# Kernel optimization log

Hardware: AMD Instinct MI355X
Metric: run time of the kernel (lower is better)

Reference implementation:

```python
import jax, jax.numpy as jnp
import numpy as np

T, D, F, FS, E = 2048, 1024, 2048, 2048, 8
TOP_K = 1


def setup_inputs() -> dict:
    key = jax.random.key(0)
    ks = jax.random.split(key, 8)
    sd = 1.0 / np.sqrt(D)
    sf = 1.0 / np.sqrt(F)
    sfs = 1.0 / np.sqrt(FS)
    return {
        "hidden_states": jax.random.normal(ks[0], (T, D), jnp.float32),
        "router_w": jax.random.normal(ks[1], (E, D), jnp.float32) * sd,     # Linear(D->E), no bias
        "w_gate": jax.random.normal(ks[2], (E, D, F), jnp.float32) * sd,    # fused gate half
        "w_up": jax.random.normal(ks[3], (E, D, F), jnp.float32) * sd,      # fused up half
        "w_down": jax.random.normal(ks[4], (E, F, D), jnp.float32) * sf,
        "ws_gate": jax.random.normal(ks[5], (D, FS), jnp.float32) * sd,
        "ws_up": jax.random.normal(ks[6], (D, FS), jnp.float32) * sd,
        "ws_down": jax.random.normal(ks[7], (FS, D), jnp.float32) * sfs,
    }


def reference(hidden_states, router_w, w_gate, w_up, w_down, ws_gate, ws_up, ws_down):
    # Router: logits -> top-k -> sigmoid of top-k values (Llama4RenormalizeMoeRoutingMethod)
    logits = hidden_states @ router_w.T                      # [T, E]
    top_vals, top_idx = jax.lax.top_k(logits, TOP_K)         # [T, K]
    scores = jax.nn.sigmoid(top_vals.astype(jnp.float32)).astype(hidden_states.dtype)
    # Combine weights [T, E]; apply_router_weight_on_input=True -> scale INPUT per routed copy
    combine = (jax.nn.one_hot(top_idx, E, dtype=hidden_states.dtype) * scores[..., None]).sum(axis=1)
    xe = combine.T[:, :, None] * hidden_states[None]          # [E, T, D] (zero for non-routed tokens)
    g = jnp.einsum('etd,edf->etf', xe, w_gate)
    u = jnp.einsum('etd,edf->etf', xe, w_up)
    routed = jnp.einsum('etf,efd->etd', jax.nn.silu(g) * u, w_down).sum(axis=0)  # [T, D]
    # Shared expert (GatedMLP, SiLU)
    shared = (jax.nn.silu(hidden_states @ ws_gate) * (hidden_states @ ws_up)) @ ws_down
    return shared + routed
```

## Files before the change

kernel.cpp:

```cpp
#include <hip/hip_runtime.h>
#include <hip/hip_bf16.h>
#include <cstdint>
#include <cstddef>

#define T_TOK 2048
#define DIM   1024
#define FDIM  2048
#define NEXP  8
#define BSTRIDE 40

#define GU_MAX 96
#define DN_MAX 96

typedef short  short8  __attribute__((ext_vector_type(8)));
typedef float  floatx4 __attribute__((ext_vector_type(4)));

__device__ inline unsigned short f2bf(float f) {
    unsigned int u = __builtin_bit_cast(unsigned int, f);
    unsigned int r = (u + 0x7FFFu + ((u >> 16) & 1u)) >> 16;
    return (unsigned short)r;
}

__global__ __launch_bounds__(256) void k_router(
    const float* __restrict__ h, const float* __restrict__ rw,
    int* __restrict__ counts, int* __restrict__ lists,
    unsigned short* __restrict__ hb, unsigned short* __restrict__ xb)
{
    int w = threadIdx.x >> 6, lane = threadIdx.x & 63;
    int t = blockIdx.x * 4 + w;
    const float* hrow = h + (size_t)t * DIM;
    float hv[16];
    #pragma unroll
    for (int i = 0; i < 16; ++i) hv[i] = hrow[lane + 64 * i];
    float acc[NEXP];
    #pragma unroll
    for (int e = 0; e < NEXP; ++e) {
        const float* r = rw + (size_t)e * DIM;
        float s = 0.f;
        #pragma unroll
        for (int i = 0; i < 16; ++i) s += hv[i] * r[lane + 64 * i];
        acc[e] = s;
    }
    #pragma unroll
    for (int e = 0; e < NEXP; ++e) {
        float s = acc[e];
        for (int off = 32; off > 0; off >>= 1) s += __shfl_down(s, off);
        acc[e] = s;
    }
    float score = 0.f;
    if (lane == 0) {
        int be = 0; float bv = acc[0];
        #pragma unroll
        for (int e = 1; e < NEXP; ++e) if (acc[e] > bv) { bv = acc[e]; be = e; }
        score = 1.f / (1.f + __expf(-bv));
        int pos = atomicAdd(&counts[be], 1);
        lists[be * T_TOK + pos] = t;
    }
    score = __shfl(score, 0);
    unsigned short* hbr = hb + (size_t)t * DIM;
    unsigned short* xbr = xb + (size_t)t * DIM;
    #pragma unroll
    for (int i = 0; i < 16; ++i) {
        hbr[lane + 64 * i] = f2bf(hv[i]);
        xbr[lane + 64 * i] = f2bf(score * hv[i]);
    }
}

__global__ void k_schedule(const int* __restrict__ counts,
                           int* __restrict__ gu, int* __restrict__ dn)
{
    if (threadIdx.x != 0 || blockIdx.x != 0) return;
    int n = 0;
    for (int e = 0; e < NEXP; ++e) {
        int c = counts[e];
        for (int r = 0; r < c; r += 64) gu[n++] = (e << 16) | r;
    }
    for (int r = 0; r < T_TOK; r += 64) gu[n++] = (NEXP << 16) | r;
    while (n < GU_MAX) gu[n++] = -1;
    n = 0;
    for (int e = 0; e < NEXP; ++e) {
        int c = counts[e];
        for (int r = 0; r < c; r += 64) {
            dn[n++] = (e << 16) | r;
            dn[n++] = (1 << 28) | (e << 16) | r;
        }
    }
    while (n < DN_MAX) dn[n++] = -1;
}

__global__ __launch_bounds__(256) void k_gateup(
    const unsigned short* __restrict__ xb, const unsigned short* __restrict__ hb,
    const float* __restrict__ w_gate, const float* __restrict__ w_up,
    const float* __restrict__ ws_gate, const float* __restrict__ ws_up,
    const int* __restrict__ counts, const int* __restrict__ lists,
    const int* __restrict__ gu_tiles, unsigned short* __restrict__ Hc)
{
    int ent = gu_tiles[blockIdx.y];
    if (ent < 0) return;
    int e = ent >> 16, row0 = ent & 0xffff;
    bool sh = (e == NEXP);
    int cnt = sh ? T_TOK : counts[e];
    const unsigned short* Asrc = sh ? hb : xb;
    const float* Bg = sh ? ws_gate : w_gate + (size_t)e * DIM * FDIM;
    const float* Bu = sh ? ws_up   : w_up   + (size_t)e * DIM * FDIM;
    int outoff = sh ? FDIM : 0;
    int col0 = blockIdx.x * 128;

    __shared__ int toks[64];
    __shared__ __align__(16) unsigned short As [64  * BSTRIDE];
    __shared__ __align__(16) unsigned short Bgs[128 * BSTRIDE];
    __shared__ __align__(16) unsigned short Bus[128 * BSTRIDE];

    int tid = threadIdx.x;
    if (tid < 64) {
        int r = row0 + tid;
        toks[tid] = (r < cnt) ? (sh ? r : lists[e * T_TOK + r]) : -1;
    }
    __syncthreads();

    int lane = tid & 63, w = tid >> 6;
    int wm = w >> 1, wn = w & 1;
    int arow = tid >> 2, aq = tid & 3;
    int atok = toks[arow];

    floatx4 accg[2][4], accu[2][4];
    #pragma unroll
    for (int mi = 0; mi < 2; ++mi)
    #pragma unroll
    for (int ni = 0; ni < 4; ++ni) {
        floatx4 z = {0.f, 0.f, 0.f, 0.f};
        accg[mi][ni] = z; accu[mi][ni] = z;
    }

    uint4 pa;
    float gr[2][8], ur[2][8];
    auto prefetch = [&](int k0) {
        pa = make_uint4(0u, 0u, 0u, 0u);
        if (atok >= 0) pa = *(const uint4*)(Asrc + (size_t)atok * DIM + k0 + aq * 8);
        #pragma unroll
        for (int it = 0; it < 2; ++it) {
            int tt = tid + it * 256;
            int n = tt & 127, kg = tt >> 7;
            const float* pg = Bg + (size_t)(k0 + kg * 8) * FDIM + col0 + n;
            const float* pu = Bu + (size_t)(k0 + kg * 8) * FDIM + col0 + n;
            #pragma unroll
            for (int j = 0; j < 8; ++j) {
                gr[it][j] = pg[(size_t)j * FDIM];
                ur[it][j] = pu[(size_t)j * FDIM];
            }
        }
    };
    auto commit = [&]() {
        *(uint4*)&As[arow * BSTRIDE + aq * 8] = pa;
        #pragma unroll
        for (int it = 0; it < 2; ++it) {
            int tt = tid + it * 256;
            int n = tt & 127, kg = tt >> 7;
            unsigned int gw[4], uw[4];
            #pragma unroll
            for (int j = 0; j < 4; ++j) {
                gw[j] = (unsigned)f2bf(gr[it][2*j]) | ((unsigned)f2bf(gr[it][2*j+1]) << 16);
                uw[j] = (unsigned)f2bf(ur[it][2*j]) | ((unsigned)f2bf(ur[it][2*j+1]) << 16);
            }
            *(uint4*)&Bgs[n * BSTRIDE + kg * 8] = make_uint4(gw[0], gw[1], gw[2], gw[3]);
            *(uint4*)&Bus[n * BSTRIDE + kg * 8] = make_uint4(uw[0], uw[1], uw[2], uw[3]);
        }
    };

    prefetch(0);
    for (int k0 = 0; k0 < DIM; k0 += 32) {
        __syncthreads();
        commit();
        if (k0 + 32 < DIM) prefetch(k0 + 32);
        __syncthreads();

        int kb = (lane >> 4) * 8;
        short8 a[2], bg[4], bu[4];
        #pragma unroll
        for (int mi = 0; mi < 2; ++mi) {
            int m = wm * 32 + mi * 16 + (lane & 15);
            a[mi] = *(const short8*)&As[m * BSTRIDE + kb];
        }
        #pragma unroll
        for (int ni = 0; ni < 4; ++ni) {
            int n = wn * 64 + ni * 16 + (lane & 15);
            bg[ni] = *(const short8*)&Bgs[n * BSTRIDE + kb];
            bu[ni] = *(const short8*)&Bus[n * BSTRIDE + kb];
        }
        #pragma unroll
        for (int mi = 0; mi < 2; ++mi)
        #pragma unroll
        for (int ni = 0; ni < 4; ++ni) {
            accg[mi][ni] = __builtin_amdgcn_mfma_f32_16x16x32_bf16(a[mi], bg[ni], accg[mi][ni], 0, 0, 0);
            accu[mi][ni] = __builtin_amdgcn_mfma_f32_16x16x32_bf16(a[mi], bu[ni], accu[mi][ni], 0, 0, 0);
        }
    }

    #pragma unroll
    for (int mi = 0; mi < 2; ++mi)
    #pragma unroll
    for (int ni = 0; ni < 4; ++ni)
    #pragma unroll
    for (int r = 0; r < 4; ++r) {
        int row = wm * 32 + mi * 16 + (lane >> 4) * 4 + r;
        int tok = toks[row];
        if (tok < 0) continue;
        int col = col0 + wn * 64 + ni * 16 + (lane & 15);
        float g = accg[mi][ni][r], u = accu[mi][ni][r];
        float hval = (g / (1.f + __expf(-g))) * u;
        Hc[(size_t)tok * (2 * FDIM) + outoff + col] = f2bf(hval);
    }
}

__global__ __launch_bounds__(256) void k_down(
    const unsigned short* __restrict__ Hc,
    const float* __restrict__ w_down, const float* __restrict__ ws_down,
    const int* __restrict__ counts, const int* __restrict__ lists,
    const int* __restrict__ dn_tiles, float* __restrict__ out)
{
    int ent = dn_tiles[blockIdx.y];
    if (ent < 0) return;
    int ks = (ent >> 28) & 1, e = (ent >> 16) & 0xff, row0 = ent & 0xffff;
    int cnt = counts[e];
    const float* B = ks ? ws_down : w_down + (size_t)e * FDIM * DIM;
    int col0 = blockIdx.x * 128;

    __shared__ int toks[64];
    __shared__ __align__(16) unsigned short As[64  * BSTRIDE];
    __shared__ __align__(16) unsigned short Bs[128 * BSTRIDE];

    int tid = threadIdx.x;
    if (tid < 64) {
        int r = row0 + tid;
        toks[tid] = (r < cnt) ? lists[e * T_TOK + r] : -1;
    }
    __syncthreads();

    int lane = tid & 63, w = tid >> 6;
    int wm = w >> 1, wn = w & 1;
    int arow = tid >> 2, aq = tid & 3;
    int atok = toks[arow];
    size_t abase = (size_t)ks * FDIM;

    floatx4 acc[2][4];
    #pragma unroll
    for (int mi = 0; mi < 2; ++mi)
    #pragma unroll
    for (int ni = 0; ni < 4; ++ni) {
        floatx4 z = {0.f, 0.f, 0.f, 0.f};
        acc[mi][ni] = z;
    }

    uint4 pa;
    float br[2][8];
    auto prefetch = [&](int k0) {
        pa = make_uint4(0u, 0u, 0u, 0u);
        if (atok >= 0)
            pa = *(const uint4*)(Hc + (size_t)atok * (2 * FDIM) + abase + k0 + aq * 8);
        #pragma unroll
        for (int it = 0; it < 2; ++it) {
            int tt = tid + it * 256;
            int n = tt & 127, kg = tt >> 7;
            const float* pb = B + (size_t)(k0 + kg * 8) * DIM + col0 + n;
            #pragma unroll
            for (int j = 0; j < 8; ++j) br[it][j] = pb[(size_t)j * DIM];
        }
    };
    auto commit = [&]() {
        *(uint4*)&As[arow * BSTRIDE + aq * 8] = pa;
        #pragma unroll
        for (int it = 0; it < 2; ++it) {
            int tt = tid + it * 256;
            int n = tt & 127, kg = tt >> 7;
            unsigned int bw[4];
            #pragma unroll
            for (int j = 0; j < 4; ++j)
                bw[j] = (unsigned)f2bf(br[it][2*j]) | ((unsigned)f2bf(br[it][2*j+1]) << 16);
            *(uint4*)&Bs[n * BSTRIDE + kg * 8] = make_uint4(bw[0], bw[1], bw[2], bw[3]);
        }
    };

    prefetch(0);
    for (int k0 = 0; k0 < FDIM; k0 += 32) {
        __syncthreads();
        commit();
        if (k0 + 32 < FDIM) prefetch(k0 + 32);
        __syncthreads();

        int kb = (lane >> 4) * 8;
        short8 a[2], b[4];
        #pragma unroll
        for (int mi = 0; mi < 2; ++mi) {
            int m = wm * 32 + mi * 16 + (lane & 15);
            a[mi] = *(const short8*)&As[m * BSTRIDE + kb];
        }
        #pragma unroll
        for (int ni = 0; ni < 4; ++ni) {
            int n = wn * 64 + ni * 16 + (lane & 15);
            b[ni] = *(const short8*)&Bs[n * BSTRIDE + kb];
        }
        #pragma unroll
        for (int mi = 0; mi < 2; ++mi)
        #pragma unroll
        for (int ni = 0; ni < 4; ++ni)
            acc[mi][ni] = __builtin_amdgcn_mfma_f32_16x16x32_bf16(a[mi], b[ni], acc[mi][ni], 0, 0, 0);
    }

    #pragma unroll
    for (int mi = 0; mi < 2; ++mi)
    #pragma unroll
    for (int ni = 0; ni < 4; ++ni)
    #pragma unroll
    for (int r = 0; r < 4; ++r) {
        int row = wm * 32 + mi * 16 + (lane >> 4) * 4 + r;
        int tok = toks[row];
        if (tok < 0) continue;
        int col = col0 + wn * 64 + ni * 16 + (lane & 15);
        atomicAdd(&out[(size_t)tok * DIM + col], acc[mi][ni][r]);
    }
}

extern "C" void kernel_launch(void* const* d_in, const int* in_sizes, int n_in,
                              void* d_out, int out_size, void* d_ws, size_t ws_size,
                              hipStream_t stream)
{
    const float* h   = (const float*)d_in[0];
    const float* rw  = (const float*)d_in[1];
    const float* wg  = (const float*)d_in[2];
    const float* wu  = (const float*)d_in[3];
    const float* wd  = (const float*)d_in[4];
    const float* wsg = (const float*)d_in[5];
    const float* wsu = (const float*)d_in[6];
    const float* wsd = (const float*)d_in[7];
    float* out = (float*)d_out;

    char* ws = (char*)d_ws;
    int* counts   = (int*)ws;
    int* gu_tiles = (int*)(ws + 256);
    int* dn_tiles = (int*)(ws + 1024);
    int* lists    = (int*)(ws + 2048);
    unsigned short* hb = (unsigned short*)(ws + 131072);
    unsigned short* xb = hb + (size_t)T_TOK * DIM;
    unsigned short* Hc = xb + (size_t)T_TOK * DIM;

    hipMemsetAsync(counts, 0, 64, stream);
    hipMemsetAsync(out, 0, (size_t)T_TOK * DIM * sizeof(float), stream);
    k_router<<<dim3(T_TOK / 4), 256, 0, stream>>>(h, rw, counts, lists, hb, xb);
    k_schedule<<<dim3(1), 64, 0, stream>>>(counts, gu_tiles, dn_tiles);
    k_gateup<<<dim3(FDIM / 128, GU_MAX), 256, 0, stream>>>(
        xb, hb, wg, wu, wsg, wsu, counts, lists, gu_tiles, Hc);
    k_down<<<dim3(DIM / 128, DN_MAX), 256, 0, stream>>>(
        Hc, wd, wsd, counts, lists, dn_tiles, out);
}
```

Baseline: 415.9 us.

## Pre-convert weights to transposed bf16 and load tiles via global_load_lds

Adds per-call kernels that convert and transpose the fp32 expert and shared weights into bf16 K-contiguous buffers. The GEMM kernels then stream A and B tiles straight into LDS with global_load_lds, using an XOR swizzle instead of padding. The M tile grows from 64 to 128 tokens. The goal is to remove strided fp32 loads and per-tile conversion from the GEMM inner loops and to raise reuse of the weights. In exchange, each call adds an extra full read and write pass over every weight, and the new loop has a single LDS buffer with no overlap between loading and compute.

```diff
diff --git a/kernel.cpp b/kernel.cpp
--- a/kernel.cpp
+++ b/kernel.cpp
@@ -7,10 +7,9 @@
 #define DIM   1024
 #define FDIM  2048
 #define NEXP  8
-#define BSTRIDE 40
-
-#define GU_MAX 96
-#define DN_MAX 96
+
+#define GU_MAX 64
+#define DN_MAX 64
 
 typedef short  short8  __attribute__((ext_vector_type(8)));
 typedef float  floatx4 __attribute__((ext_vector_type(4)));
@@ -21,6 +20,12 @@
     return (unsigned short)r;
 }
 
+__device__ inline void glds16(const void* g, void* l) {
+    __builtin_amdgcn_global_load_lds(
+        (const __attribute__((address_space(1))) unsigned int*)g,
+        (__attribute__((address_space(3))) unsigned int*)l, 16, 0, 0);
+}
+
 __global__ __launch_bounds__(256) void k_router(
     const float* __restrict__ h, const float* __restrict__ rw,
     int* __restrict__ counts, int* __restrict__ lists,
@@ -73,14 +78,14 @@
     int n = 0;
     for (int e = 0; e < NEXP; ++e) {
         int c = counts[e];
-        for (int r = 0; r < c; r += 64) gu[n++] = (e << 16) | r;
-    }
-    for (int r = 0; r < T_TOK; r += 64) gu[n++] = (NEXP << 16) | r;
+        for (int r = 0; r < c; r += 128) gu[n++] = (e << 16) | r;
+    }
+    for (int r = 0; r < T_TOK; r += 128) gu[n++] = (NEXP << 16) | r;
     while (n < GU_MAX) gu[n++] = -1;
     n = 0;
     for (int e = 0; e < NEXP; ++e) {
         int c = counts[e];
-        for (int r = 0; r < c; r += 64) {
+        for (int r = 0; r < c; r += 128) {
             dn[n++] = (e << 16) | r;
             dn[n++] = (1 << 28) | (e << 16) | r;
         }
@@ -88,10 +93,59 @@
     while (n < DN_MAX) dn[n++] = -1;
 }
 
+__global__ __launch_bounds__(256) void k_cvt_gu(
+    const float* __restrict__ wg, const float* __restrict__ wu,
+    const float* __restrict__ wsg, const float* __restrict__ wsu,
+    unsigned short* __restrict__ wgT, unsigned short* __restrict__ wuT,
+    unsigned short* __restrict__ wsgT, unsigned short* __restrict__ wsuT)
+{
+    int z = blockIdx.y;
+    const float* src; unsigned short* dst;
+    if (z < NEXP)        { src = wg + (size_t)z * DIM * FDIM;          dst = wgT + (size_t)z * FDIM * DIM; }
+    else if (z < 2*NEXP) { src = wu + (size_t)(z - NEXP) * DIM * FDIM; dst = wuT + (size_t)(z - NEXP) * FDIM * DIM; }
+    else if (z == 2*NEXP){ src = wsg; dst = wsgT; }
+    else                 { src = wsu; dst = wsuT; }
+    int n  = blockIdx.x * 64 + (threadIdx.x >> 2);
+    int kg = (threadIdx.x & 3) * 8;
+    for (int k0 = 0; k0 < DIM; k0 += 32) {
+        int k = k0 + kg;
+        float v[8];
+        #pragma unroll
+        for (int j = 0; j < 8; ++j) v[j] = src[(size_t)(k + j) * FDIM + n];
+        unsigned int p[4];
+        #pragma unroll
+        for (int j = 0; j < 4; ++j)
+            p[j] = (unsigned)f2bf(v[2*j]) | ((unsigned)f2bf(v[2*j+1]) << 16);
+        *(uint4*)&dst[(size_t)n * DIM + k] = make_uint4(p[0], p[1], p[2], p[3]);
+    }
+}
+
+__global__ __launch_bounds__(256) void k_cvt_dn(
+    const float* __restrict__ wd, const float* __restrict__ wsd,
+    unsigned short* __restrict__ wdT, unsigned short* __restrict__ wsdT)
+{
+    int z = blockIdx.y;
+    const float* src = (z < NEXP) ? wd + (size_t)z * FDIM * DIM : wsd;
+    unsigned short* dst = (z < NEXP) ? wdT + (size_t)z * DIM * FDIM : wsdT;
+    int n  = blockIdx.x * 64 + (threadIdx.x >> 2);
+    int kg = (threadIdx.x & 3) * 8;
+    for (int k0 = 0; k0 < FDIM; k0 += 32) {
+        int k = k0 + kg;
+        float v[8];
+        #pragma unroll
+        for (int j = 0; j < 8; ++j) v[j] = src[(size_t)(k + j) * DIM + n];
+        unsigned int p[4];
+        #pragma unroll
+        for (int j = 0; j < 4; ++j)
+            p[j] = (unsigned)f2bf(v[2*j]) | ((unsigned)f2bf(v[2*j+1]) << 16);
+        *(uint4*)&dst[(size_t)n * FDIM + k] = make_uint4(p[0], p[1], p[2], p[3]);
+    }
+}
+
 __global__ __launch_bounds__(256) void k_gateup(
     const unsigned short* __restrict__ xb, const unsigned short* __restrict__ hb,
-    const float* __restrict__ w_gate, const float* __restrict__ w_up,
-    const float* __restrict__ ws_gate, const float* __restrict__ ws_up,
+    const unsigned short* __restrict__ wgT, const unsigned short* __restrict__ wuT,
+    const unsigned short* __restrict__ wsgT, const unsigned short* __restrict__ wsuT,
     const int* __restrict__ counts, const int* __restrict__ lists,
     const int* __restrict__ gu_tiles, unsigned short* __restrict__ Hc)
 {
@@ -101,18 +155,18 @@
     bool sh = (e == NEXP);
     int cnt = sh ? T_TOK : counts[e];
     const unsigned short* Asrc = sh ? hb : xb;
-    const float* Bg = sh ? ws_gate : w_gate + (size_t)e * DIM * FDIM;
-    const float* Bu = sh ? ws_up   : w_up   + (size_t)e * DIM * FDIM;
+    const unsigned short* Bg = sh ? wsgT : wgT + (size_t)e * FDIM * DIM;
+    const unsigned short* Bu = sh ? wsuT : wuT + (size_t)e * FDIM * DIM;
     int outoff = sh ? FDIM : 0;
     int col0 = blockIdx.x * 128;
 
-    __shared__ int toks[64];
-    __shared__ __align__(16) unsigned short As [64  * BSTRIDE];
-    __shared__ __align__(16) unsigned short Bgs[128 * BSTRIDE];
-    __shared__ __align__(16) unsigned short Bus[128 * BSTRIDE];
+    __shared__ int toks[128];
+    __shared__ __align__(16) unsigned short As [128 * 32];
+    __shared__ __align__(16) unsigned short Bgs[128 * 32];
+    __shared__ __align__(16) unsigned short Bus[128 * 32];
 
     int tid = threadIdx.x;
-    if (tid < 64) {
+    if (tid < 128) {
         int r = row0 + tid;
         toks[tid] = (r < cnt) ? (sh ? r : lists[e * T_TOK + r]) : -1;
     }
@@ -120,89 +174,69 @@
 
     int lane = tid & 63, w = tid >> 6;
     int wm = w >> 1, wn = w & 1;
-    int arow = tid >> 2, aq = tid & 3;
-    int atok = toks[arow];
-
-    floatx4 accg[2][4], accu[2][4];
-    #pragma unroll
-    for (int mi = 0; mi < 2; ++mi)
+
+    int rw_[2], kg_[2], atk[2];
+    #pragma unroll
+    for (int it = 0; it < 2; ++it) {
+        int tt = tid + it * 256;
+        int rr = tt >> 2, sq = tt & 3;
+        rw_[it] = rr;
+        kg_[it] = (sq ^ ((rr >> 1) & 3)) * 8;
+        int tk = toks[rr];
+        atk[it] = tk < 0 ? 0 : tk;
+    }
+
+    floatx4 accg[4][4], accu[4][4];
+    #pragma unroll
+    for (int mi = 0; mi < 4; ++mi)
     #pragma unroll
     for (int ni = 0; ni < 4; ++ni) {
         floatx4 z = {0.f, 0.f, 0.f, 0.f};
         accg[mi][ni] = z; accu[mi][ni] = z;
     }
 
-    uint4 pa;
-    float gr[2][8], ur[2][8];
-    auto prefetch = [&](int k0) {
-        pa = make_uint4(0u, 0u, 0u, 0u);
-        if (atok >= 0) pa = *(const uint4*)(Asrc + (size_t)atok * DIM + k0 + aq * 8);
-        #pragma unroll
-        for (int it = 0; it < 2; ++it) {
-            int tt = tid + it * 256;
-            int n = tt & 127, kg = tt >> 7;
-            const float* pg = Bg + (size_t)(k0 + kg * 8) * FDIM + col0 + n;
-            const float* pu = Bu + (size_t)(k0 + kg * 8) * FDIM + col0 + n;
-            #pragma unroll
-            for (int j = 0; j < 8; ++j) {
-                gr[it][j] = pg[(size_t)j * FDIM];
-                ur[it][j] = pu[(size_t)j * FDIM];
-            }
-        }
-    };
-    auto commit = [&]() {
-        *(uint4*)&As[arow * BSTRIDE + aq * 8] = pa;
-        #pragma unroll
-        for (int it = 0; it < 2; ++it) {
-            int tt = tid + it * 256;
-            int n = tt & 127, kg = tt >> 7;
-            unsigned int gw[4], uw[4];
-            #pragma unroll
-            for (int j = 0; j < 4; ++j) {
-                gw[j] = (unsigned)f2bf(gr[it][2*j]) | ((unsigned)f2bf(gr[it][2*j+1]) << 16);
-                uw[j] = (unsigned)f2bf(ur[it][2*j]) | ((unsigned)f2bf(ur[it][2*j+1]) << 16);
-            }
-            *(uint4*)&Bgs[n * BSTRIDE + kg * 8] = make_uint4(gw[0], gw[1], gw[2], gw[3]);
-            *(uint4*)&Bus[n * BSTRIDE + kg * 8] = make_uint4(uw[0], uw[1], uw[2], uw[3]);
-        }
-    };
-
-    prefetch(0);
     for (int k0 = 0; k0 < DIM; k0 += 32) {
         __syncthreads();
-        commit();
-        if (k0 + 32 < DIM) prefetch(k0 + 32);
+        #pragma unroll
+        for (int it = 0; it < 2; ++it) {
+            int loff = (tid + it * 256) * 8;
+            glds16(Asrc + (size_t)atk[it] * DIM + k0 + kg_[it], &As[loff]);
+            glds16(Bg + (size_t)(col0 + rw_[it]) * DIM + k0 + kg_[it], &Bgs[loff]);
+            glds16(Bu + (size_t)(col0 + rw_[it]) * DIM + k0 + kg_[it], &Bus[loff]);
+        }
         __syncthreads();
 
         int kb = (lane >> 4) * 8;
-        short8 a[2], bg[4], bu[4];
-        #pragma unroll
-        for (int mi = 0; mi < 2; ++mi) {
-            int m = wm * 32 + mi * 16 + (lane & 15);
-            a[mi] = *(const short8*)&As[m * BSTRIDE + kb];
+        short8 af[4], bgf[4], buf_[4];
+        #pragma unroll
+        for (int mi = 0; mi < 4; ++mi) {
+            int r = wm * 64 + mi * 16 + (lane & 15);
+            int slot = (((kb >> 3) ^ ((r >> 1) & 3))) * 8;
+            af[mi] = *(const short8*)&As[r * 32 + slot];
         }
         #pragma unroll
         for (int ni = 0; ni < 4; ++ni) {
             int n = wn * 64 + ni * 16 + (lane & 15);
-            bg[ni] = *(const short8*)&Bgs[n * BSTRIDE + kb];
-            bu[ni] = *(const short8*)&Bus[n * BSTRIDE + kb];
-        }
-        #pragma unroll
-        for (int mi = 0; mi < 2; ++mi)
+            int slot = (((kb >> 3) ^ ((n >> 1) & 3))) * 8;
+            bgf[ni]  = *(const short8*)&Bgs[n * 32 + slot];
+            buf_[ni] = *(const short8*)&Bus[n * 32 + slot];
+        }
+        #pragma unroll
+        for (int mi = 0; mi < 4; ++mi)
         #pragma unroll
         for (int ni = 0; ni < 4; ++ni) {
-            accg[mi][ni] = __builtin_amdgcn_mfma_f32_16x16x32_bf16(a[mi], bg[ni], accg[mi][ni], 0, 0, 0);
-            accu[mi][ni] = __builtin_amdgcn_mfma_f32_16x16x32_bf16(a[mi], bu[ni], accu[mi][ni], 0, 0, 0);
-        }
-    }
-
-    #pragma unroll
-    for (int mi = 0; mi < 2; ++mi)
+            accg[mi][ni] = __builtin_amdgcn_mfma_f32_16x16x32_bf16(af[mi], bgf[ni],  accg[mi][ni], 0, 0, 0);
+            accu[mi][ni] = __builtin_amdgcn_mfma_f32_16x16x32_bf16(af[mi], buf_[ni], accu[mi][ni], 0, 0, 0);
+        }
+    }
+
+    #pragma unroll
+    for (int mi = 0; mi < 4; ++mi)
     #pragma unroll
     for (int ni = 0; ni < 4; ++ni)
     #pragma unroll
     for (int r = 0; r < 4; ++r) {
-        int row = wm * 32 + mi * 16 + (lane >> 4) * 4 + r;
+        int row = wm * 64 + mi * 16 + (lane >> 4) * 4 + r;
         int tok = toks[row];
         if (tok < 0) continue;
         int col = col0 + wn * 64 + ni * 16 + (lane & 15);
@@ -214,7 +248,7 @@
 
 __global__ __launch_bounds__(256) void k_down(
     const unsigned short* __restrict__ Hc,
-    const float* __restrict__ w_down, const float* __restrict__ ws_down,
+    const unsigned short* __restrict__ wdT, const unsigned short* __restrict__ wsdT,
     const int* __restrict__ counts, const int* __restrict__ lists,
     const int* __restrict__ dn_tiles, float* __restrict__ out)
 {
@@ -222,15 +256,16 @@
     if (ent < 0) return;
     int ks = (ent >> 28) & 1, e = (ent >> 16) & 0xff, row0 = ent & 0xffff;
     int cnt = counts[e];
-    const float* B = ks ? ws_down : w_down + (size_t)e * FDIM * DIM;
+    const unsigned short* B = ks ? wsdT : wdT + (size_t)e * DIM * FDIM;
     int col0 = blockIdx.x * 128;
-
-    __shared__ int toks[64];
-    __shared__ __align__(16) unsigned short As[64  * BSTRIDE];
-    __shared__ __align__(16) unsigned short Bs[128 * BSTRIDE];
+    size_t abase = (size_t)ks * FDIM;
+
+    __shared__ int toks[128];
+    __shared__ __align__(16) unsigned short As[128 * 32];
+    __shared__ __align__(16) unsigned short Bs[128 * 32];
 
     int tid = threadIdx.x;
-    if (tid < 64) {
+    if (tid < 128) {
         int r = row0 + tid;
         toks[tid] = (r < cnt) ? lists[e * T_TOK + r] : -1;
     }
@@ -238,81 +273,65 @@
 
     int lane = tid & 63, w = tid >> 6;
     int wm = w >> 1, wn = w & 1;
-    int arow = tid >> 2, aq = tid & 3;
-    int atok = toks[arow];
-    size_t abase = (size_t)ks * FDIM;
-
-    floatx4 acc[2][4];
-    #pragma unroll
-    for (int mi = 0; mi < 2; ++mi)
+
+    int rw_[2], kg_[2], atk[2];
+    #pragma unroll
+    for (int it = 0; it < 2; ++it) {
+        int tt = tid + it * 256;
+        int rr = tt >> 2, sq = tt & 3;
+        rw_[it] = rr;
+        kg_[it] = (sq ^ ((rr >> 1) & 3)) * 8;
+        int tk = toks[rr];
+        atk[it] = tk < 0 ? 0 : tk;
+    }
+
+    floatx4 acc[4][4];
+    #pragma unroll
+    for (int mi = 0; mi < 4; ++mi)
     #pragma unroll
     for (int ni = 0; ni < 4; ++ni) {
         floatx4 z = {0.f, 0.f, 0.f, 0.f};
         acc[mi][ni] = z;
     }
 
-    uint4 pa;
-    float br[2][8];
-    auto prefetch = [&](int k0) {
-        pa = make_uint4(0u, 0u, 0u, 0u);
-        if (atok >= 0)
-            pa = *(const uint4*)(Hc + (size_t)atok * (2 * FDIM) + abase + k0 + aq * 8);
-        #pragma unroll
-        for (int it = 0; it < 2; ++it) {
-            int tt = tid + it * 256;
-            int n = tt & 127, kg = tt >> 7;
-            const float* pb = B + (size_t)(k0 + kg * 8) * DIM + col0 + n;
-            #pragma unroll
-            for (int j = 0; j < 8; ++j) br[it][j] = pb[(size_t)j * DIM];
-        }
-    };
-    auto commit = [&]() {
-        *(uint4*)&As[arow * BSTRIDE + aq * 8] = pa;
-        #pragma unroll
-        for (int it = 0; it < 2; ++it) {
-            int tt = tid + it * 256;
-            int n = tt & 127, kg = tt >> 7;
-            unsigned int bw[4];
-            #pragma unroll
-            for (int j = 0; j < 4; ++j)
-                bw[j] = (unsigned)f2bf(br[it][2*j]) | ((unsigned)f2bf(br[it][2*j+1]) << 16);
-            *(uint4*)&Bs[n * BSTRIDE + kg * 8] = make_uint4(bw[0], bw[1], bw[2], bw[3]);
-        }
-    };
-
-    prefetch(0);
     for (int k0 = 0; k0 < FDIM; k0 += 32) {
         __syncthreads();
-        commit();
-        if (k0 + 32 < FDIM) prefetch(k0 + 32);
+        #pragma unroll
+        for (int it = 0; it < 2; ++it) {
+            int loff = (tid + it * 256) * 8;
+            glds16(Hc + (size_t)atk[it] * (2 * FDIM) + abase + k0 + kg_[it], &As[loff]);
+            glds16(B + (size_t)(col0 + rw_[it]) * FDIM + k0 + kg_[it], &Bs[loff]);
+        }
         __syncthreads();
 
         int kb = (lane >> 4) * 8;
-        short8 a[2], b[4];
-        #pragma unroll
-        for (int mi = 0; mi < 2; ++mi) {
-            int m = wm * 32 + mi * 16 + (lane & 15);
-            a[mi] = *(const short8*)&As[m * BSTRIDE + kb];
+        short8 af[4], bf[4];
+        #pragma unroll
+        for (int mi = 0; mi < 4; ++mi) {
+            int r = wm * 64 + mi * 16 + (lane & 15);
+            int slot = (((kb >> 3) ^ ((r >> 1) & 3))) * 8;
+            af[mi] = *(const short8*)&As[r * 32 + slot];
         }
         #pragma unroll
         for (int ni = 0; ni < 4; ++ni) {
             int n = wn * 64 + ni * 16 + (lane & 15);
-            b[ni] = *(const short8*)&Bs[n * BSTRIDE + kb];
-        }
-        #pragma unroll
-        for (int mi = 0; mi < 2; ++mi)
+            int slot = (((kb >> 3) ^ ((n >> 1) & 3))) * 8;
+            bf[ni] = *(const short8*)&Bs[n * 32 + slot];
+        }
+        #pragma unroll
+        for (int mi = 0; mi < 4; ++mi)
         #pragma unroll
         for (int ni = 0; ni < 4; ++ni)
-            acc[mi][ni] = __builtin_amdgcn_mfma_f32_16x16x32_bf16(a[mi], b[ni], acc[mi][ni], 0, 0, 0);
-    }
-
-    #pragma unroll
-    for (int mi = 0; mi < 2; ++mi)
+            acc[mi][ni] = __builtin_amdgcn_mfma_f32_16x16x32_bf16(af[mi], bf[ni], acc[mi][ni], 0, 0, 0);
+    }
+
+    #pragma unroll
+    for (int mi = 0; mi < 4; ++mi)
     #pragma unroll
     for (int ni = 0; ni < 4; ++ni)
     #pragma unroll
     for (int r = 0; r < 4; ++r) {
-        int row = wm * 32 + mi * 16 + (lane >> 4) * 4 + r;
+        int row = wm * 64 + mi * 16 + (lane >> 4) * 4 + r;
         int tok = toks[row];
         if (tok < 0) continue;
         int col = col0 + wn * 64 + ni * 16 + (lane & 15);
@@ -334,21 +353,32 @@
     const float* wsd = (const float*)d_in[7];
     float* out = (float*)d_out;
 
+    const size_t MB = 1024 * 1024;
     char* ws = (char*)d_ws;
     int* counts   = (int*)ws;
     int* gu_tiles = (int*)(ws + 256);
     int* dn_tiles = (int*)(ws + 1024);
     int* lists    = (int*)(ws + 2048);
-    unsigned short* hb = (unsigned short*)(ws + 131072);
-    unsigned short* xb = hb + (size_t)T_TOK * DIM;
-    unsigned short* Hc = xb + (size_t)T_TOK * DIM;
+    unsigned short* hb  = (unsigned short*)(ws + 131072);
+    unsigned short* xb  = (unsigned short*)(ws + 131072 + 4*MB);
+    unsigned short* Hc  = (unsigned short*)(ws + 131072 + 8*MB);
+    char* W = ws + 131072 + 24 * MB;
+    unsigned short* wgT  = (unsigned short*)(W);
+    unsigned short* wuT  = (unsigned short*)(W + 32*MB);
+    unsigned short* wsgT = (unsigned short*)(W + 64*MB);
+    unsigned short* wsuT = (unsigned short*)(W + 68*MB);
+    unsigned short* wdT  = (unsigned short*)(W);
+    unsigned short* wsdT = (unsigned short*)(W + 32*MB);
 
     hipMemsetAsync(counts, 0, 64, stream);
     hipMemsetAsync(out, 0, (size_t)T_TOK * DIM * sizeof(float), stream);
+    k_cvt_gu<<<dim3(FDIM / 64, 2 * NEXP + 2), 256, 0, stream>>>(
+        wg, wu, wsg, wsu, wgT, wuT, wsgT, wsuT);
     k_router<<<dim3(T_TOK / 4), 256, 0, stream>>>(h, rw, counts, lists, hb, xb);
     k_schedule<<<dim3(1), 64, 0, stream>>>(counts, gu_tiles, dn_tiles);
     k_gateup<<<dim3(FDIM / 128, GU_MAX), 256, 0, stream>>>(
-        xb, hb, wg, wu, wsg, wsu, counts, lists, gu_tiles, Hc);
+        xb, hb, wgT, wuT, wsgT, wsuT, counts, lists, gu_tiles, Hc);
+    k_cvt_dn<<<dim3(DIM / 64, NEXP + 1), 256, 0, stream>>>(wd, wsd, wdT, wsdT);
     k_down<<<dim3(DIM / 128, DN_MAX), 256, 0, stream>>>(
-        Hc, wd, wsd, counts, lists, dn_tiles, out);
-}
+        Hc, wdT, wsdT, counts, lists, dn_tiles, out);
+}
```

New measurement: 531.1 us. 27.7% more time.

## Enlarge M tiles, double-buffer LDS with direct global-to-LDS loads and XOR swizzle

Applied to the files above, without the earlier changes.

Row tiles in the gate/up and down GEMMs grow from 64 to 128 tokens, and the down kernel's column tile shrinks to 64. Each weight tile loaded from global memory is therefore reused across more tokens. LDS becomes double-buffered with one barrier per k-step, activations are copied global-to-LDS with buffer_load...lds, and padded strides are replaced by an XOR swizzle to avoid bank conflicts. The cost is higher register use (launch_bounds 256,2) and more padding waste on small experts. DN_MAX=64 may be too small if routing is very uneven, since small partial tiles per expert could overflow it.

```diff
diff --git a/kernel.cpp b/kernel.cpp
--- a/kernel.cpp
+++ b/kernel.cpp
@@ -7,10 +7,9 @@
 #define DIM   1024
 #define FDIM  2048
 #define NEXP  8
-#define BSTRIDE 40
-
-#define GU_MAX 96
-#define DN_MAX 96
+
+#define GU_MAX 48
+#define DN_MAX 64
 
 typedef short  short8  __attribute__((ext_vector_type(8)));
 typedef float  floatx4 __attribute__((ext_vector_type(4)));
@@ -21,6 +20,17 @@
     return (unsigned short)r;
 }
 
+__device__ inline unsigned int pk2bf(float a, float b) {
+    return (unsigned int)f2bf(a) | ((unsigned int)f2bf(b) << 16);
+}
+
+__device__ inline void glds16(const void* g, const unsigned short* lds_base, int elem_off) {
+    int u = __builtin_amdgcn_readfirstlane(elem_off);
+    __builtin_amdgcn_global_load_lds(
+        (const __attribute__((address_space(1))) unsigned int*)g,
+        (__attribute__((address_space(3))) unsigned int*)(lds_base + u), 16, 0, 0);
+}
+
 __global__ __launch_bounds__(256) void k_router(
     const float* __restrict__ h, const float* __restrict__ rw,
     int* __restrict__ counts, int* __restrict__ lists,
@@ -73,14 +83,14 @@
     int n = 0;
     for (int e = 0; e < NEXP; ++e) {
         int c = counts[e];
-        for (int r = 0; r < c; r += 64) gu[n++] = (e << 16) | r;
-    }
-    for (int r = 0; r < T_TOK; r += 64) gu[n++] = (NEXP << 16) | r;
+        for (int r = 0; r < c; r += 128) gu[n++] = (e << 16) | r;
+    }
+    for (int r = 0; r < T_TOK; r += 128) gu[n++] = (NEXP << 16) | r;
     while (n < GU_MAX) gu[n++] = -1;
     n = 0;
     for (int e = 0; e < NEXP; ++e) {
         int c = counts[e];
-        for (int r = 0; r < c; r += 64) {
+        for (int r = 0; r < c; r += 128) {
             dn[n++] = (e << 16) | r;
             dn[n++] = (1 << 28) | (e << 16) | r;
         }
@@ -88,7 +98,7 @@
     while (n < DN_MAX) dn[n++] = -1;
 }
 
-__global__ __launch_bounds__(256) void k_gateup(
+__global__ __launch_bounds__(256, 2) void k_gateup(
     const unsigned short* __restrict__ xb, const unsigned short* __restrict__ hb,
     const float* __restrict__ w_gate, const float* __restrict__ w_up,
     const float* __restrict__ ws_gate, const float* __restrict__ ws_up,
@@ -106,13 +116,13 @@
     int outoff = sh ? FDIM : 0;
     int col0 = blockIdx.x * 128;
 
-    __shared__ int toks[64];
-    __shared__ __align__(16) unsigned short As [64  * BSTRIDE];
-    __shared__ __align__(16) unsigned short Bgs[128 * BSTRIDE];
-    __shared__ __align__(16) unsigned short Bus[128 * BSTRIDE];
+    __shared__ int toks[128];
+    __shared__ __align__(16) unsigned short As [2][128 * 32];
+    __shared__ __align__(16) unsigned short Bgs[2][128 * 32];
+    __shared__ __align__(16) unsigned short Bus[2][128 * 32];
 
     int tid = threadIdx.x;
-    if (tid < 64) {
+    if (tid < 128) {
         int r = row0 + tid;
         toks[tid] = (r < cnt) ? (sh ? r : lists[e * T_TOK + r]) : -1;
     }
@@ -120,89 +130,109 @@
 
     int lane = tid & 63, w = tid >> 6;
     int wm = w >> 1, wn = w & 1;
-    int arow = tid >> 2, aq = tid & 3;
-    int atok = toks[arow];
-
-    floatx4 accg[2][4], accu[2][4];
-    #pragma unroll
-    for (int mi = 0; mi < 2; ++mi)
+
+    size_t agoff[2]; int albase[2];
+    #pragma unroll
+    for (int it = 0; it < 2; ++it) {
+        int tt = tid + it * 256;
+        int rr = tt >> 2, sq = tt & 3;
+        int kg = (sq ^ ((rr >> 1) & 3)) * 8;
+        int tk = toks[rr]; if (tk < 0) tk = 0;
+        agoff[it] = (size_t)tk * DIM + kg;
+        albase[it] = (it * 256 + w * 64) * 8;
+    }
+
+    int c = tid & 63;
+    int kq = w;
+    int slotB = (kq ^ (c & 3)) * 8;
+    const float* bgp = Bg + (size_t)(kq * 8) * FDIM + col0 + 2 * c;
+    const float* bup = Bu + (size_t)(kq * 8) * FDIM + col0 + 2 * c;
+
+    float2 gx[8], ux[8];
+    auto loadB = [&](int k0) {
+        const float* pg = bgp + (size_t)k0 * FDIM;
+        const float* pu = bup + (size_t)k0 * FDIM;
+        #pragma unroll
+        for (int j = 0; j < 8; ++j) {
+            gx[j] = *(const float2*)(pg + (size_t)j * FDIM);
+            ux[j] = *(const float2*)(pu + (size_t)j * FDIM);
+        }
+    };
+    auto commitB = [&](int p) {
+        unsigned int ge[4], go[4], ue[4], uo[4];
+        #pragma unroll
+        for (int j = 0; j < 4; ++j) {
+            ge[j] = pk2bf(gx[2*j].x, gx[2*j+1].x);
+            go[j] = pk2bf(gx[2*j].y, gx[2*j+1].y);
+            ue[j] = pk2bf(ux[2*j].x, ux[2*j+1].x);
+            uo[j] = pk2bf(ux[2*j].y, ux[2*j+1].y);
+        }
+        *(uint4*)&Bgs[p][(2*c)   * 32 + slotB] = make_uint4(ge[0], ge[1], ge[2], ge[3]);
+        *(uint4*)&Bgs[p][(2*c+1) * 32 + slotB] = make_uint4(go[0], go[1], go[2], go[3]);
+        *(uint4*)&Bus[p][(2*c)   * 32 + slotB] = make_uint4(ue[0], ue[1], ue[2], ue[3]);
+        *(uint4*)&Bus[p][(2*c+1) * 32 + slotB] = make_uint4(uo[0], uo[1], uo[2], uo[3]);
+    };
+    auto loadA = [&](int k0, int p) {
+        #pragma unroll
+        for (int it = 0; it < 2; ++it)
+            glds16(Asrc + agoff[it] + k0, &As[p][0], albase[it]);
+    };
+
+    floatx4 accg[4][4], accu[4][4];
+    #pragma unroll
+    for (int mi = 0; mi < 4; ++mi)
     #pragma unroll
     for (int ni = 0; ni < 4; ++ni) {
         floatx4 z = {0.f, 0.f, 0.f, 0.f};
         accg[mi][ni] = z; accu[mi][ni] = z;
     }
 
-    uint4 pa;
-    float gr[2][8], ur[2][8];
-    auto prefetch = [&](int k0) {
-        pa = make_uint4(0u, 0u, 0u, 0u);
-        if (atok >= 0) pa = *(const uint4*)(Asrc + (size_t)atok * DIM + k0 + aq * 8);
-        #pragma unroll
-        for (int it = 0; it < 2; ++it) {
-            int tt = tid + it * 256;
-            int n = tt & 127, kg = tt >> 7;
-            const float* pg = Bg + (size_t)(k0 + kg * 8) * FDIM + col0 + n;
-            const float* pu = Bu + (size_t)(k0 + kg * 8) * FDIM + col0 + n;
-            #pragma unroll
-            for (int j = 0; j < 8; ++j) {
-                gr[it][j] = pg[(size_t)j * FDIM];
-                ur[it][j] = pu[(size_t)j * FDIM];
-            }
-        }
-    };
-    auto commit = [&]() {
-        *(uint4*)&As[arow * BSTRIDE + aq * 8] = pa;
-        #pragma unroll
-        for (int it = 0; it < 2; ++it) {
-            int tt = tid + it * 256;
-            int n = tt & 127, kg = tt >> 7;
-            unsigned int gw[4], uw[4];
-            #pragma unroll
-            for (int j = 0; j < 4; ++j) {
-                gw[j] = (unsigned)f2bf(gr[it][2*j]) | ((unsigned)f2bf(gr[it][2*j+1]) << 16);
-                uw[j] = (unsigned)f2bf(ur[it][2*j]) | ((unsigned)f2bf(ur[it][2*j+1]) << 16);
-            }
-            *(uint4*)&Bgs[n * BSTRIDE + kg * 8] = make_uint4(gw[0], gw[1], gw[2], gw[3]);
-            *(uint4*)&Bus[n * BSTRIDE + kg * 8] = make_uint4(uw[0], uw[1], uw[2], uw[3]);
-        }
-    };
-
-    prefetch(0);
+    loadA(0, 0);
+    loadB(0);
+    commitB(0);
+    loadB(32);
+
+    int p = 0;
     for (int k0 = 0; k0 < DIM; k0 += 32) {
         __syncthreads();
-        commit();
-        if (k0 + 32 < DIM) prefetch(k0 + 32);
-        __syncthreads();
-
+        int nk = k0 + 32;
+        if (nk < DIM) {
+            loadA(nk, p ^ 1);
+            commitB(p ^ 1);
+            if (nk + 32 < DIM) loadB(nk + 32);
+        }
         int kb = (lane >> 4) * 8;
-        short8 a[2], bg[4], bu[4];
-        #pragma unroll
-        for (int mi = 0; mi < 2; ++mi) {
-            int m = wm * 32 + mi * 16 + (lane & 15);
-            a[mi] = *(const short8*)&As[m * BSTRIDE + kb];
+        short8 af[4], bgf[4], buf_[4];
+        #pragma unroll
+        for (int mi = 0; mi < 4; ++mi) {
+            int r = wm * 64 + mi * 16 + (lane & 15);
+            int slot = ((kb >> 3) ^ ((r >> 1) & 3)) * 8;
+            af[mi] = *(const short8*)&As[p][r * 32 + slot];
         }
         #pragma unroll
         for (int ni = 0; ni < 4; ++ni) {
             int n = wn * 64 + ni * 16 + (lane & 15);
-            bg[ni] = *(const short8*)&Bgs[n * BSTRIDE + kb];
-            bu[ni] = *(const short8*)&Bus[n * BSTRIDE + kb];
-        }
-        #pragma unroll
-        for (int mi = 0; mi < 2; ++mi)
+            int slot = ((kb >> 3) ^ ((n >> 1) & 3)) * 8;
+            bgf[ni]  = *(const short8*)&Bgs[p][n * 32 + slot];
+            buf_[ni] = *(const short8*)&Bus[p][n * 32 + slot];
+        }
+        #pragma unroll
+        for (int mi = 0; mi < 4; ++mi)
         #pragma unroll
         for (int ni = 0; ni < 4; ++ni) {
-            accg[mi][ni] = __builtin_amdgcn_mfma_f32_16x16x32_bf16(a[mi], bg[ni], accg[mi][ni], 0, 0, 0);
-            accu[mi][ni] = __builtin_amdgcn_mfma_f32_16x16x32_bf16(a[mi], bu[ni], accu[mi][ni], 0, 0, 0);
-        }
-    }
-
-    #pragma unroll
-    for (int mi = 0; mi < 2; ++mi)
+            accg[mi][ni] = __builtin_amdgcn_mfma_f32_16x16x32_bf16(af[mi], bgf[ni],  accg[mi][ni], 0, 0, 0);
+            accu[mi][ni] = __builtin_amdgcn_mfma_f32_16x16x32_bf16(af[mi], buf_[ni], accu[mi][ni], 0, 0, 0);
+        }
+        p ^= 1;
+    }
+
+    #pragma unroll
+    for (int mi = 0; mi < 4; ++mi)
     #pragma unroll
     for (int ni = 0; ni < 4; ++ni)
     #pragma unroll
     for (int r = 0; r < 4; ++r) {
-        int row = wm * 32 + mi * 16 + (lane >> 4) * 4 + r;
+        int row = wm * 64 + mi * 16 + (lane >> 4) * 4 + r;
         int tok = toks[row];
         if (tok < 0) continue;
         int col = col0 + wn * 64 + ni * 16 + (lane & 15);
@@ -223,14 +253,15 @@
     int ks = (ent >> 28) & 1, e = (ent >> 16) & 0xff, row0 = ent & 0xffff;
     int cnt = counts[e];
     const float* B = ks ? ws_down : w_down + (size_t)e * FDIM * DIM;
-    int col0 = blockIdx.x * 128;
-
-    __shared__ int toks[64];
-    __shared__ __align__(16) unsigned short As[64  * BSTRIDE];
-    __shared__ __align__(16) unsigned short Bs[128 * BSTRIDE];
+    int col0 = blockIdx.x * 64;
+    size_t abase = (size_t)ks * FDIM;
+
+    __shared__ int toks[128];
+    __shared__ __align__(16) unsigned short As[2][128 * 32];
+    __shared__ __align__(16) unsigned short Bs[2][64 * 32];
 
     int tid = threadIdx.x;
-    if (tid < 64) {
+    if (tid < 128) {
         int r = row0 + tid;
         toks[tid] = (r < cnt) ? lists[e * T_TOK + r] : -1;
     }
@@ -238,84 +269,96 @@
 
     int lane = tid & 63, w = tid >> 6;
     int wm = w >> 1, wn = w & 1;
-    int arow = tid >> 2, aq = tid & 3;
-    int atok = toks[arow];
-    size_t abase = (size_t)ks * FDIM;
-
-    floatx4 acc[2][4];
-    #pragma unroll
-    for (int mi = 0; mi < 2; ++mi)
-    #pragma unroll
-    for (int ni = 0; ni < 4; ++ni) {
+
+    size_t agoff[2]; int albase[2];
+    #pragma unroll
+    for (int it = 0; it < 2; ++it) {
+        int tt = tid + it * 256;
+        int rr = tt >> 2, sq = tt & 3;
+        int kg = (sq ^ ((rr >> 1) & 3)) * 8;
+        int tk = toks[rr]; if (tk < 0) tk = 0;
+        agoff[it] = (size_t)tk * (2 * FDIM) + abase + kg;
+        albase[it] = (it * 256 + w * 64) * 8;
+    }
+
+    int c = tid & 63;
+    int kq = w;
+    int slotB = (kq ^ ((c >> 1) & 3)) * 8;
+    const float* bp = B + (size_t)(kq * 8) * DIM + col0 + c;
+
+    float bx[8];
+    auto loadB = [&](int k0) {
+        const float* pb = bp + (size_t)k0 * DIM;
+        #pragma unroll
+        for (int j = 0; j < 8; ++j) bx[j] = pb[(size_t)j * DIM];
+    };
+    auto commitB = [&](int p) {
+        unsigned int bw[4];
+        #pragma unroll
+        for (int j = 0; j < 4; ++j) bw[j] = pk2bf(bx[2*j], bx[2*j+1]);
+        *(uint4*)&Bs[p][c * 32 + slotB] = make_uint4(bw[0], bw[1], bw[2], bw[3]);
+    };
+    auto loadA = [&](int k0, int p) {
+        #pragma unroll
+        for (int it = 0; it < 2; ++it)
+            glds16(Hc + agoff[it] + k0, &As[p][0], albase[it]);
+    };
+
+    floatx4 acc[4][2];
+    #pragma unroll
+    for (int mi = 0; mi < 4; ++mi)
+    #pragma unroll
+    for (int ni = 0; ni < 2; ++ni) {
         floatx4 z = {0.f, 0.f, 0.f, 0.f};
         acc[mi][ni] = z;
     }
 
-    uint4 pa;
-    float br[2][8];
-    auto prefetch = [&](int k0) {
-        pa = make_uint4(0u, 0u, 0u, 0u);
-        if (atok >= 0)
-            pa = *(const uint4*)(Hc + (size_t)atok * (2 * FDIM) + abase + k0 + aq * 8);
-        #pragma unroll
-        for (int it = 0; it < 2; ++it) {
-            int tt = tid + it * 256;
-            int n = tt & 127, kg = tt >> 7;
-            const float* pb = B + (size_t)(k0 + kg * 8) * DIM + col0 + n;
-            #pragma unroll
-            for (int j = 0; j < 8; ++j) br[it][j] = pb[(size_t)j * DIM];
-        }
-    };
-    auto commit = [&]() {
-        *(uint4*)&As[arow * BSTRIDE + aq * 8] = pa;
-        #pragma unroll
-        for (int it = 0; it < 2; ++it) {
-            int tt = tid + it * 256;
-            int n = tt & 127, kg = tt >> 7;
-            unsigned int bw[4];
-            #pragma unroll
-            for (int j = 0; j < 4; ++j)
-                bw[j] = (unsigned)f2bf(br[it][2*j]) | ((unsigned)f2bf(br[it][2*j+1]) << 16);
-            *(uint4*)&Bs[n * BSTRIDE + kg * 8] = make_uint4(bw[0], bw[1], bw[2], bw[3]);
-        }
-    };
-
-    prefetch(0);
+    loadA(0, 0);
+    loadB(0);
+    commitB(0);
+    loadB(32);
+
+    int p = 0;
     for (int k0 = 0; k0 < FDIM; k0 += 32) {
         __syncthreads();
-        commit();
-        if (k0 + 32 < FDIM) prefetch(k0 + 32);
-        __syncthreads();
-
+        int nk = k0 + 32;
+        if (nk < FDIM) {
+            loadA(nk, p ^ 1);
+            commitB(p ^ 1);
+            if (nk + 32 < FDIM) loadB(nk + 32);
+        }
         int kb = (lane >> 4) * 8;
-        short8 a[2], b[4];
-        #pragma unroll
-        for (int mi = 0; mi < 2; ++mi) {
-            int m = wm * 32 + mi * 16 + (lane & 15);
-            a[mi] = *(const short8*)&As[m * BSTRIDE + kb];
-        }
-        #pragma unroll
-        for (int ni = 0; ni < 4; ++ni) {
-            int n = wn * 64 + ni * 16 + (lane & 15);
-            b[ni] = *(const short8*)&Bs[n * BSTRIDE + kb];
-        }
-        #pragma unroll
-        for (int mi = 0; mi < 2; ++mi)
-        #pragma unroll
-        for (int ni = 0; ni < 4; ++ni)
-            acc[mi][ni] = __builtin_amdgcn_mfma_f32_16x16x32_bf16(a[mi], b[ni], acc[mi][ni], 0, 0, 0);
-    }
-
-    #pragma unroll
-    for (int mi = 0; mi < 2; ++mi)
-    #pragma unroll
-    for (int ni = 0; ni < 4; ++ni)
+        short8 af[4], bf[2];
+        #pragma unroll
+        for (int mi = 0; mi < 4; ++mi) {
+            int r = wm * 64 + mi * 16 + (lane & 15);
+            int slot = ((kb >> 3) ^ ((r >> 1) & 3)) * 8;
+            af[mi] = *(const short8*)&As[p][r * 32 + slot];
+        }
+        #pragma unroll
+        for (int ni = 0; ni < 2; ++ni) {
+            int n = wn * 32 + ni * 16 + (lane & 15);
+            int slot = ((kb >> 3) ^ ((n >> 1) & 3)) * 8;
+            bf[ni] = *(const short8*)&Bs[p][n * 32 + slot];
+        }
+        #pragma unroll
+        for (int mi = 0; mi < 4; ++mi)
+        #pragma unroll
+        for (int ni = 0; ni < 2; ++ni)
+            acc[mi][ni] = __builtin_amdgcn_mfma_f32_16x16x32_bf16(af[mi], bf[ni], acc[mi][ni], 0, 0, 0);
+        p ^= 1;
+    }
+
+    #pragma unroll
+    for (int mi = 0; mi < 4; ++mi)
+    #pragma unroll
+    for (int ni = 0; ni < 2; ++ni)
     #pragma unroll
     for (int r = 0; r < 4; ++r) {
-        int row = wm * 32 + mi * 16 + (lane >> 4) * 4 + r;
+        int row = wm * 64 + mi * 16 + (lane >> 4) * 4 + r;
         int tok = toks[row];
         if (tok < 0) continue;
-        int col = col0 + wn * 64 + ni * 16 + (lane & 15);
+        int col = col0 + wn * 32 + ni * 16 + (lane & 15);
         atomicAdd(&out[(size_t)tok * DIM + col], acc[mi][ni][r]);
     }
 }
@@ -343,12 +386,12 @@
     unsigned short* xb = hb + (size_t)T_TOK * DIM;
     unsigned short* Hc = xb + (size_t)T_TOK * DIM;
 
-    hipMemsetAsync(counts, 0, 64, stream);
-    hipMemsetAsync(out, 0, (size_t)T_TOK * DIM * sizeof(float), stream);
+    (void)hipMemsetAsync(counts, 0, 64, stream);
+    (void)hipMemsetAsync(out, 0, (size_t)T_TOK * DIM * sizeof(float), stream);
     k_router<<<dim3(T_TOK / 4), 256, 0, stream>>>(h, rw, counts, lists, hb, xb);
     k_schedule<<<dim3(1), 64, 0, stream>>>(counts, gu_tiles, dn_tiles);
     k_gateup<<<dim3(FDIM / 128, GU_MAX), 256, 0, stream>>>(
         xb, hb, wg, wu, wsg, wsu, counts, lists, gu_tiles, Hc);
-    k_down<<<dim3(DIM / 128, DN_MAX), 256, 0, stream>>>(
+    k_down<<<dim3(DIM / 64, DN_MAX), 256, 0, stream>>>(
         Hc, wd, wsd, counts, lists, dn_tiles, out);
 }
```

Measured after the change: 414.0 us. No clear change (-0.5%).
